# Optimization experiments

Hardware: AMD Instinct MI355X
Metric: run time of the kernel (lower is better)

## Reference

```python
import jax, jax.numpy as jnp
import numpy as np
import math

D_MODEL = 1024
N_HEADS = 16
D_K = D_MODEL // N_HEADS
MAX_LEN = 200
B, S = 64, 200


def _temporal_bias():
    # bias[i, j] = -0.1 * |i - j| / max_len, same for every head
    idx = jnp.arange(MAX_LEN, dtype=jnp.float32)
    dist = jnp.abs(idx[:, None] - idx[None, :])  # [L, L]
    tb = (-0.1 * dist / MAX_LEN)[None, None, :, :]  # [1, 1, L, L]
    return jnp.broadcast_to(tb, (1, N_HEADS, MAX_LEN, MAX_LEN))


def setup_inputs() -> dict:
    key = jax.random.key(0)
    ks = jax.random.split(key, 9)
    lim = 1.0 / math.sqrt(D_MODEL)
    def lin_w(k):
        return jax.random.uniform(k, (D_MODEL, D_MODEL), jnp.float32, -lim, lim)
    def lin_b(k):
        return jax.random.uniform(k, (D_MODEL,), jnp.float32, -lim, lim)
    return {
        "x": jax.random.normal(ks[0], (B, S, D_MODEL), jnp.float32),
        "mask": jnp.ones((B, 1, S, S), jnp.int32),
        "wq": lin_w(ks[1]), "bq": lin_b(ks[2]),
        "wk": lin_w(ks[3]), "bk": lin_b(ks[4]),
        "wv": lin_w(ks[5]), "bv": lin_b(ks[6]),
        "wo": lin_w(ks[7]), "bo": lin_b(ks[8]),
        "temporal_bias": _temporal_bias(),
    }


def reference(x, mask, wq, bq, wk, bk, wv, bv, wo, bo, temporal_bias):
    b, s, d = x.shape
    h, dk = N_HEADS, D_K
    scale = math.sqrt(dk)
    # torch Linear: y = x @ W.T + b; heads: [b, s, h, dk] -> [b, h, s, dk]
    q = (jnp.einsum('bsd,ed->bse', x, wq) + bq).reshape(b, s, h, dk).transpose(0, 2, 1, 3)
    k = (jnp.einsum('bsd,ed->bse', x, wk) + bk).reshape(b, s, h, dk).transpose(0, 2, 1, 3)
    v = (jnp.einsum('bsd,ed->bse', x, wv) + bv).reshape(b, s, h, dk).transpose(0, 2, 1, 3)
    scores = jnp.einsum('bhqd,bhkd->bhqk', q, k) / scale  # [b, h, s, s]
    scores = scores + temporal_bias[:, :, :s, :s]
    scores = jnp.where(mask == 0, jnp.float32(-1e9), scores)
    attn = jax.nn.softmax(scores, axis=-1)  # dropout is identity in eval mode
    ctx = jnp.einsum('bhqk,bhkd->bhqd', attn, v)
    ctx = ctx.transpose(0, 2, 1, 3).reshape(b, s, d)
    out = jnp.einsum('bsd,ed->bse', ctx, wo) + bo
    return out, attn
```

## Files before the change

### kernel.cpp

```cpp
#include <hip/hip_runtime.h>
#include <stdint.h>

typedef unsigned short u16;
typedef unsigned long long u64;
typedef __bf16 bf16x8 __attribute__((ext_vector_type(8)));
typedef float f32x4 __attribute__((ext_vector_type(4)));

#define MFMA16(a, b, c) __builtin_amdgcn_mfma_f32_16x16x32_bf16((a), (b), (c), 0, 0, 0)

#define BB 64
#define SS 200
#define DM 1024
#define NH 16
#define MM (BB * SS)
#define OUT0_ELEMS (MM * DM)

__device__ static inline u16 f2bf(float f) {
    __bf16 h = (__bf16)f;
    return __builtin_bit_cast(u16, h);
}

__device__ static inline bf16x8 load8(const u16* p) {
    uint4 u = *(const uint4*)p;
    union { uint4 u; bf16x8 b; } cv; cv.u = u; return cv.b;
}

__device__ static inline bf16x8 bzero8() {
    union { uint4 u; bf16x8 b; } cv; cv.u = make_uint4(0u, 0u, 0u, 0u); return cv.b;
}

__device__ static inline void gload_lds16(const void* g, void* l) {
    __builtin_amdgcn_global_load_lds(
        (const __attribute__((address_space(1))) void*)g,
        (__attribute__((address_space(3))) void*)l, 16, 0, 0);
}

__global__ __launch_bounds__(256) void convert_k(
    const float* __restrict__ x,
    const float* __restrict__ wq, const float* __restrict__ wk,
    const float* __restrict__ wv, const float* __restrict__ wo,
    u16* __restrict__ xb,
    u16* __restrict__ wqb, u16* __restrict__ wkb,
    u16* __restrict__ wvb, u16* __restrict__ wob)
{
    size_t i4 = (size_t)blockIdx.x * 256 + threadIdx.x;
    size_t e = i4 * 4;
    const float* src; u16* dst; size_t off;
    if (e < (size_t)OUT0_ELEMS) { src = x; dst = xb; off = e; }
    else {
        size_t we = e - OUT0_ELEMS;
        size_t w = we >> 20;
        off = we & 1048575u;
        src = (w == 0) ? wq : (w == 1) ? wk : (w == 2) ? wv : wo;
        dst = (w == 0) ? wqb : (w == 1) ? wkb : (w == 2) ? wvb : wob;
    }
    float4 v = *(const float4*)(src + off);
    union { u16 s[4]; uint2 u; } o;
    o.s[0] = f2bf(v.x); o.s[1] = f2bf(v.y); o.s[2] = f2bf(v.z); o.s[3] = f2bf(v.w);
    *(uint2*)(dst + off) = o.u;
}

__global__ __launch_bounds__(256) void maskbits_k(
    const int* __restrict__ mask, u64* __restrict__ bits)
{
    __shared__ unsigned char nb[4][64];
    const int wave = threadIdx.x >> 6, lane = threadIdx.x & 63;
    const int row = blockIdx.x * 4 + wave;
    const int* mp = mask + (size_t)row * 200;
    unsigned nib;
    if (lane < 50) {
        int4 v = *(const int4*)(mp + lane * 4);
        nib = (v.x ? 1u : 0u) | (v.y ? 2u : 0u) | (v.z ? 4u : 0u) | (v.w ? 8u : 0u);
    } else nib = 0xFu;
    nb[wave][lane] = (unsigned char)nib;
    __builtin_amdgcn_s_waitcnt(0);
    if (lane < 4) {
        const unsigned char* p = &nb[wave][lane * 16];
        u64 m = 0;
#pragma unroll
        for (int i = 0; i < 16; i++) m |= (u64)(p[i] & 0xFu) << (4 * i);
        bits[(size_t)row * 4 + lane] = m;
    }
}

template <int MODE>
__global__ __launch_bounds__(256) void gemm_k(
    const u16* __restrict__ A, const u16* __restrict__ W,
    const float* __restrict__ b0, const float* __restrict__ b1, const float* __restrict__ b2,
    u16* __restrict__ qo, u16* __restrict__ ko, u16* __restrict__ vto,
    float* __restrict__ outf)
{
    __shared__ __align__(16) u16 sm[8192];
    u16* As = sm;
    u16* Bs = sm + 4096;

    const int tid  = threadIdx.x;
    const int wave = tid >> 6;
    const int lane = tid & 63;
    const int quad = lane >> 4;
    const int l15  = lane & 15;
    const int n0   = blockIdx.x * 128;
    const int m0   = blockIdx.y * 128;
    const int seg  = (MODE == 0) ? (n0 >> 10) : 0;
    const int nn0  = n0 & 1023;
    const float* bias = (MODE == 1) ? b0 : (seg == 0 ? b0 : (seg == 1 ? b1 : b2));

    const int srow = wave * 16 + (lane >> 2);
    const int sk8  = (lane & 3) * 8;
    const int wuni = __builtin_amdgcn_readfirstlane(wave);

    f32x4 acc[4][4];
#pragma unroll
    for (int i = 0; i < 4; i++)
#pragma unroll
        for (int j = 0; j < 4; j++) acc[i][j] = (f32x4){0.f, 0.f, 0.f, 0.f};

    const int wr = (wave >> 1) * 64;
    const int wc = (wave & 1) * 64;

    const u16* Ag = A + (size_t)m0 * 1024;
    const u16* Wg = W + (size_t)n0 * 1024;

    for (int kc = 0; kc < 1024; kc += 32) {
        __syncthreads();
#pragma unroll
        for (int r = 0; r < 2; r++) {
            int row = r * 64 + srow;
            gload_lds16(Ag + (size_t)row * 1024 + kc + sk8, &As[(r * 64 + wuni * 16) * 32]);
        }
#pragma unroll
        for (int r = 0; r < 2; r++) {
            int row = r * 64 + srow;
            gload_lds16(Wg + (size_t)row * 1024 + kc + sk8, &Bs[(r * 64 + wuni * 16) * 32]);
        }
        __syncthreads();

        bf16x8 af[4], bf[4];
#pragma unroll
        for (int mt = 0; mt < 4; mt++) af[mt] = load8(&As[(wr + mt * 16 + l15) * 32 + quad * 8]);
#pragma unroll
        for (int nt = 0; nt < 4; nt++) bf[nt] = load8(&Bs[(wc + nt * 16 + l15) * 32 + quad * 8]);
#pragma unroll
        for (int mt = 0; mt < 4; mt++)
#pragma unroll
            for (int nt = 0; nt < 4; nt++)
                acc[mt][nt] = MFMA16(af[mt], bf[nt], acc[mt][nt]);
    }

    if (MODE == 1) {
#pragma unroll
        for (int nt = 0; nt < 4; nt++) {
            int n = n0 + wc + nt * 16 + l15;
            float bv = bias[n];
#pragma unroll
            for (int mt = 0; mt < 4; mt++)
#pragma unroll
                for (int r = 0; r < 4; r++) {
                    int m = m0 + wr + mt * 16 + quad * 4 + r;
                    __builtin_nontemporal_store(acc[mt][nt][r] + bv,
                                                &outf[(size_t)m * 1024 + n]);
                }
        }
    } else if (seg == 2) {
#pragma unroll
        for (int nt = 0; nt < 4; nt++) {
            int nn = nn0 + wc + nt * 16 + l15;
            float bv = bias[nn];
            int hh = nn >> 6, d = nn & 63;
#pragma unroll
            for (int mt = 0; mt < 4; mt++) {
                int mbase = m0 + wr + mt * 16 + quad * 4;
                int b = mbase / 200, s = mbase - b * 200;
                union { u16 q[4]; uint2 u; } pk;
#pragma unroll
                for (int r = 0; r < 4; r++) pk.q[r] = f2bf(acc[mt][nt][r] + bv);
                *(uint2*)&vto[((size_t)(b * 16 + hh) * 64 + d) * 200 + s] = pk.u;
            }
        }
    } else {
        u16* dst = (seg == 0) ? qo : ko;
        float bv[4];
#pragma unroll
        for (int nt = 0; nt < 4; nt++) bv[nt] = bias[nn0 + wc + nt * 16 + l15];
#pragma unroll
        for (int h2 = 0; h2 < 2; h2++) {
            __syncthreads();
            if ((wave >> 1) == h2) {
#pragma unroll
                for (int nt = 0; nt < 4; nt++)
#pragma unroll
                    for (int mt = 0; mt < 4; mt++)
#pragma unroll
                        for (int r = 0; r < 4; r++) {
                            int rl = mt * 16 + quad * 4 + r;
                            int c  = wc + nt * 16 + l15;
                            sm[rl * 128 + (c ^ ((rl & 7) << 4))] = f2bf(acc[mt][nt][r] + bv[nt]);
                        }
            }
            __syncthreads();
#pragma unroll
            for (int j = 0; j < 4; j++) {
                int idx = tid + j * 256;
                int rl = idx >> 4, c8 = (idx & 15) * 8;
                int c8s = c8 ^ ((rl & 7) << 4);
                uint4 vv = *(const uint4*)&sm[rl * 128 + c8s];
                *(uint4*)&dst[((size_t)(m0 + h2 * 64 + rl)) * 1024 + nn0 + c8] = vv;
            }
        }
    }
}

__global__ __launch_bounds__(256) __attribute__((amdgpu_waves_per_eu(3, 4)))
void attn_k(
    const u16* __restrict__ qg, const u16* __restrict__ kg, const u16* __restrict__ vtg,
    const u64* __restrict__ mbits,
    float* __restrict__ attn_out, u16* __restrict__ ctxb)
{
    __shared__ __align__(16) u16 Pb[4][16 * 208];

    const int tid  = threadIdx.x;
    const int wave = tid >> 6;
    const int lane = tid & 63;
    const int quad = lane >> 4;
    const int l15  = lane & 15;

    const int task = blockIdx.x * 4 + wave;
    const int bh   = task / 13;
    const int i0   = (task - bh * 13) * 16;
    const int b    = bh >> 4;
    const int h    = bh & 15;

    u16* pb = Pb[wave];

    const u16* qkbase = qg + (size_t)b * 200 * 1024 + h * 64;
    int qi = i0 + l15;
    const u16* qrow = qkbase + (size_t)(qi < 200 ? qi : 0) * 1024;
    bf16x8 aq0, aq1;
    if (qi < 200) { aq0 = load8(qrow + quad * 8); aq1 = load8(qrow + 32 + quad * 8); }
    else          { aq0 = bzero8(); aq1 = bzero8(); }

    const int ib = i0 + quad * 4;
    const u16* kbase = kg + (size_t)b * 200 * 1024 + h * 64;
    const u64* mrow = mbits + (size_t)b * 200 * 4;
    const float TBC = -0.1f / 200.0f;

#define KLOAD(T, A, B) do {                                              \
        int kj_ = (T) * 16 + l15;                                        \
        const u16* kr_ = kbase + (size_t)(kj_ < 200 ? kj_ : 0) * 1024;   \
        if (kj_ < 200) { (A) = load8(kr_ + quad * 8);                    \
                         (B) = load8(kr_ + 32 + quad * 8); }             \
        else           { (A) = bzero8(); (B) = bzero8(); }               \
    } while (0)

#define MLD(R, C) mrow[(size_t)((ib + (R)) < 200 ? (ib + (R)) : 0) * 4 + (C)]
#define LOADM(C, D) do { D[0] = MLD(0, C); D[1] = MLD(1, C);             \
                         D[2] = MLD(2, C); D[3] = MLD(3, C); } while (0)

    bf16x8 ka[4], kb4[4];
    KLOAD(0, ka[0], kb4[0]);
    KLOAD(1, ka[1], kb4[1]);
    KLOAD(2, ka[2], kb4[2]);
    KLOAD(3, ka[3], kb4[3]);

    u64 mwc[4], mwn[4];
    LOADM(0, mwc);

    f32x4 sv[13];
    f32x4 mxr = (f32x4){-3.0e38f, -3.0e38f, -3.0e38f, -3.0e38f};

#pragma unroll
    for (int t = 0; t < 13; t++) {
        bf16x8 b0 = ka[t & 3], b1 = kb4[t & 3];
        if (t + 4 < 13) KLOAD(t + 4, ka[t & 3], kb4[t & 3]);
        if ((t & 3) == 0 && (t >> 2) < 3) LOADM((t >> 2) + 1, mwn);

        f32x4 z = (f32x4){0.f, 0.f, 0.f, 0.f};
        z = MFMA16(aq0, b0, z);
        z = MFMA16(aq1, b1, z);

        const int col = t * 16 + l15;
        const int sh  = (t & 3) * 16 + l15;
        const float fc = (float)col;
        f32x4 s;
#pragma unroll
        for (int r = 0; r < 4; r++) {
            int ia = ib + r;
            float val = z[r] * 0.125f + TBC * fabsf((float)ia - fc);
            if (!((mwc[r] >> sh) & 1)) val = -1e9f;
            s[r] = (ia < 200 && col < 200) ? val : -3.0e38f;
            mxr[r] = fmaxf(mxr[r], s[r]);
        }
        sv[t] = s;

        if ((t & 3) == 3) { mwc[0] = mwn[0]; mwc[1] = mwn[1];
                            mwc[2] = mwn[2]; mwc[3] = mwn[3]; }
    }

#pragma unroll
    for (int m = 1; m < 16; m <<= 1)
#pragma unroll
        for (int r = 0; r < 4; r++)
            mxr[r] = fmaxf(mxr[r], __shfl_xor(mxr[r], m, 64));

    f32x4 sum = (f32x4){0.f, 0.f, 0.f, 0.f};
#pragma unroll
    for (int t = 0; t < 13; t++) {
        f32x4 s = sv[t];
#pragma unroll
        for (int r = 0; r < 4; r++) { s[r] = __expf(s[r] - mxr[r]); sum[r] += s[r]; }
        sv[t] = s;
    }
#pragma unroll
    for (int m = 1; m < 16; m <<= 1)
#pragma unroll
        for (int r = 0; r < 4; r++)
            sum[r] += __shfl_xor(sum[r], m, 64);

    f32x4 inv;
#pragma unroll
    for (int r = 0; r < 4; r++) inv[r] = (sum[r] > 0.f) ? 1.f / sum[r] : 0.f;

    const u16* vb = vtg + (size_t)bh * 64 * 200;
    bf16x8 vf[2][4], afr[2];

#define VLOADF(KC7, BUF) do {                                            \
        int j0v_ = (KC7) * 32 + quad * 8;                                \
        if (j0v_ < 200) {                                                \
            vf[BUF][0] = load8(vb + (0 * 16 + l15) * 200 + j0v_);        \
            vf[BUF][1] = load8(vb + (1 * 16 + l15) * 200 + j0v_);        \
            vf[BUF][2] = load8(vb + (2 * 16 + l15) * 200 + j0v_);        \
            vf[BUF][3] = load8(vb + (3 * 16 + l15) * 200 + j0v_);        \
        } else { vf[BUF][0] = bzero8(); vf[BUF][1] = bzero8();           \
                 vf[BUF][2] = bzero8(); vf[BUF][3] = bzero8(); }         \
    } while (0)
#define AFLOAD(KC7, BUF) do {                                            \
        int j0a_ = (KC7) * 32 + quad * 8;                                \
        afr[BUF] = (j0a_ < 208) ? load8(pb + l15 * 208 + j0a_) : bzero8(); \
    } while (0)

    VLOADF(0, 0);

    float* aop = attn_out + (size_t)bh * 40000;
#pragma unroll
    for (int t = 0; t < 13; t++) {
        const int col = t * 16 + l15;
#pragma unroll
        for (int r = 0; r < 4; r++) {
            int ia = ib + r;
            float a = sv[t][r] * inv[r];
            pb[(quad * 4 + r) * 208 + col] = (col < 200) ? f2bf(a) : (u16)0;
            if (ia < 200 && col < 200)
                __builtin_nontemporal_store(a, aop + (size_t)ia * 200 + col);
        }
    }

    AFLOAD(0, 0);

    f32x4 ctx[4];
#pragma unroll
    for (int nt = 0; nt < 4; nt++) ctx[nt] = (f32x4){0.f, 0.f, 0.f, 0.f};

#pragma unroll
    for (int k7 = 0; k7 < 7; k7++) {
        if (k7 < 6) { VLOADF(k7 + 1, (k7 + 1) & 1); AFLOAD(k7 + 1, (k7 + 1) & 1); }
        ctx[0] = MFMA16(afr[k7 & 1], vf[k7 & 1][0], ctx[0]);
        ctx[1] = MFMA16(afr[k7 & 1], vf[k7 & 1][1], ctx[1]);
        ctx[2] = MFMA16(afr[k7 & 1], vf[k7 & 1][2], ctx[2]);
        ctx[3] = MFMA16(afr[k7 & 1], vf[k7 & 1][3], ctx[3]);
    }

#pragma unroll
    for (int nt = 0; nt < 4; nt++)
#pragma unroll
        for (int r = 0; r < 4; r++)
            pb[(quad * 4 + r) * 208 + nt * 16 + l15] = f2bf(ctx[nt][r]);

#pragma unroll
    for (int k = 0; k < 2; k++) {
        int rr = k * 8 + (lane >> 3), ss = lane & 7;
        int ia = i0 + rr;
        uint4 val = *(const uint4*)&pb[rr * 208 + ss * 8];
        if (ia < 200)
            *(uint4*)&ctxb[((size_t)b * 200 + ia) * 1024 + h * 64 + ss * 8] = val;
    }
}

extern "C" void kernel_launch(void* const* d_in, const int* in_sizes, int n_in,
                              void* d_out, int out_size, void* d_ws, size_t ws_size,
                              hipStream_t stream) {
    const float* x    = (const float*)d_in[0];
    const int*   mask = (const int*)d_in[1];
    const float* wq   = (const float*)d_in[2];
    const float* bq   = (const float*)d_in[3];
    const float* wk   = (const float*)d_in[4];
    const float* bk   = (const float*)d_in[5];
    const float* wv   = (const float*)d_in[6];
    const float* bv   = (const float*)d_in[7];
    const float* wo   = (const float*)d_in[8];
    const float* bo   = (const float*)d_in[9];

    float* out  = (float*)d_out;
    float* attn = out + OUT0_ELEMS;

    char* ws = (char*)d_ws;
    u16* xb    = (u16*)(ws);
    u16* wqb   = (u16*)(ws + 26214400);
    u16* wkb   = (u16*)(ws + 28311552);
    u16* wvb   = (u16*)(ws + 30408704);
    u16* wob   = (u16*)(ws + 32505856);
    u16* qb    = (u16*)(ws + 34603008);
    u16* kb    = (u16*)(ws + 60817408);
    u16* vtb   = (u16*)(ws + 87031808);
    u16* ctxb  = (u16*)(ws + 113246208);
    u64* mbits = (u64*)(ws + 139460608);

    convert_k<<<dim3(16896), dim3(256), 0, stream>>>(x, wq, wk, wv, wo, xb, wqb, wkb, wvb, wob);

    maskbits_k<<<dim3(3200), dim3(256), 0, stream>>>(mask, mbits);

    gemm_k<0><<<dim3(24, 100), dim3(256), 0, stream>>>(
        xb, wqb, bq, bk, bv, qb, kb, vtb, nullptr);

    attn_k<<<dim3(3328), dim3(256), 0, stream>>>(qb, kb, vtb, mbits, attn, ctxb);

    gemm_k<1><<<dim3(8, 100), dim3(256), 0, stream>>>(
        ctxb, wob, bo, nullptr, nullptr, nullptr, nullptr, nullptr, out);
}
```

Measured before the change: 533.6 us.

## Double-buffer GEMM LDS tiles and swizzle K-chunks to avoid bank conflicts

The GEMM main loop now uses two LDS buffers, so the async global-to-LDS load of the next K chunk is issued before the MFMAs on the current chunk run. This halves the barriers per K step and overlaps memory latency with compute. It also XOR-swizzles the 8-element K offset on both the store and read side to reduce LDS bank conflicts. LDS use per block doubles to 32KB, which may lower occupancy. Correctness depends on the global-to-LDS load not overlapping reads of the same buffer, and the barrier placement appears to ensure that.

```diff
diff --git a/kernel.cpp b/kernel.cpp
--- a/kernel.cpp
+++ b/kernel.cpp
@@ -90,9 +90,11 @@
     u16* __restrict__ qo, u16* __restrict__ ko, u16* __restrict__ vto,
     float* __restrict__ outf)
 {
-    __shared__ __align__(16) u16 sm[8192];
-    u16* As = sm;
-    u16* Bs = sm + 4096;
+    __shared__ __align__(16) u16 sm[16384];
+    u16* As0 = sm;
+    u16* Bs0 = sm + 4096;
+    u16* As1 = sm + 8192;
+    u16* Bs1 = sm + 12288;
 
     const int tid  = threadIdx.x;
     const int wave = tid >> 6;
@@ -106,7 +108,8 @@
     const float* bias = (MODE == 1) ? b0 : (seg == 0 ? b0 : (seg == 1 ? b1 : b2));
 
     const int srow = wave * 16 + (lane >> 2);
-    const int sk8  = (lane & 3) * 8;
+    const int swz8 = (((lane & 3) ^ ((lane >> 3) & 3)) * 8);
+    const int rsw8 = ((quad ^ ((l15 >> 1) & 3)) * 8);
     const int wuni = __builtin_amdgcn_readfirstlane(wave);
 
     f32x4 acc[4][4];
@@ -121,30 +124,42 @@
     const u16* Ag = A + (size_t)m0 * 1024;
     const u16* Wg = W + (size_t)n0 * 1024;
 
-    for (int kc = 0; kc < 1024; kc += 32) {
+#define GSTAGE(KC, AS, BS) do {                                               \
+        gload_lds16(Ag + (size_t)srow * 1024 + (KC) + swz8,                   \
+                    &(AS)[(wuni * 16) * 32]);                                 \
+        gload_lds16(Ag + (size_t)(64 + srow) * 1024 + (KC) + swz8,            \
+                    &(AS)[(64 + wuni * 16) * 32]);                            \
+        gload_lds16(Wg + (size_t)srow * 1024 + (KC) + swz8,                   \
+                    &(BS)[(wuni * 16) * 32]);                                 \
+        gload_lds16(Wg + (size_t)(64 + srow) * 1024 + (KC) + swz8,            \
+                    &(BS)[(64 + wuni * 16) * 32]);                            \
+    } while (0)
+
+#define GCOMP(AS, BS) do {                                                    \
+        bf16x8 af_[4], bf_[4];                                                \
+        _Pragma("unroll")                                                     \
+        for (int mt = 0; mt < 4; mt++)                                        \
+            af_[mt] = load8(&(AS)[(wr + mt * 16 + l15) * 32 + rsw8]);         \
+        _Pragma("unroll")                                                     \
+        for (int nt = 0; nt < 4; nt++)                                        \
+            bf_[nt] = load8(&(BS)[(wc + nt * 16 + l15) * 32 + rsw8]);         \
+        _Pragma("unroll")                                                     \
+        for (int mt = 0; mt < 4; mt++)                                        \
+            _Pragma("unroll")                                                 \
+            for (int nt = 0; nt < 4; nt++)                                    \
+                acc[mt][nt] = MFMA16(af_[mt], bf_[nt], acc[mt][nt]);          \
+    } while (0)
+
+    GSTAGE(0, As0, Bs0);
+    __syncthreads();
+
+    for (int kc = 0; kc < 1024; kc += 64) {
+        if (kc + 32 < 1024) GSTAGE(kc + 32, As1, Bs1);
+        GCOMP(As0, Bs0);
         __syncthreads();
-#pragma unroll
-        for (int r = 0; r < 2; r++) {
-            int row = r * 64 + srow;
-            gload_lds16(Ag + (size_t)row * 1024 + kc + sk8, &As[(r * 64 + wuni * 16) * 32]);
-        }
-#pragma unroll
-        for (int r = 0; r < 2; r++) {
-            int row = r * 64 + srow;
-            gload_lds16(Wg + (size_t)row * 1024 + kc + sk8, &Bs[(r * 64 + wuni * 16) * 32]);
-        }
+        if (kc + 64 < 1024) GSTAGE(kc + 64, As0, Bs0);
+        GCOMP(As1, Bs1);
         __syncthreads();
-
-        bf16x8 af[4], bf[4];
-#pragma unroll
-        for (int mt = 0; mt < 4; mt++) af[mt] = load8(&As[(wr + mt * 16 + l15) * 32 + quad * 8]);
-#pragma unroll
-        for (int nt = 0; nt < 4; nt++) bf[nt] = load8(&Bs[(wc + nt * 16 + l15) * 32 + quad * 8]);
-#pragma unroll
-        for (int mt = 0; mt < 4; mt++)
-#pragma unroll
-            for (int nt = 0; nt < 4; nt++)
-                acc[mt][nt] = MFMA16(af[mt], bf[nt], acc[mt][nt]);
     }
 
     if (MODE == 1) {
@@ -208,6 +223,8 @@
             }
         }
     }
+#undef GSTAGE
+#undef GCOMP
 }
 
 __global__ __launch_bounds__(256) __attribute__((amdgpu_waves_per_eu(3, 4)))
```

Result: no change. 538.7 us (+1.0%).
